# Kernel tuning notes

Hardware: AMD Instinct MI355X
Metric: run time of the kernel (lower is better)

## Reference

```python
import jax, jax.numpy as jnp
import numpy as np

N, R, M, E, NE, B = 50000, 500, 120000, 960000, 800000, 8192
D, H1, HID, OC = 200, 256, 512, 50


def setup_inputs() -> dict:
    key = jax.random.key(0)
    ks = jax.random.split(key, 26)
    s = 0.05
    rn = lambda k, shp: jax.random.normal(k, shp, jnp.float32) * s
    return {
        "entity_emb": jax.random.normal(ks[0], (N, D), jnp.float32),
        "rel_emb": jax.random.normal(ks[1], (R, D), jnp.float32),
        "b_x": jax.random.randint(ks[2], (M,), 0, N),
        "b_node_graph_index": jax.random.randint(ks[3], (M,), 0, R),
        "edge_src": jax.random.randint(ks[4], (E,), 0, M),
        "edge_dst": jax.random.randint(ks[5], (E,), 0, M),
        "edge_w": jax.random.uniform(ks[6], (E,), jnp.float32),
        "big_src": jax.random.randint(ks[7], (NE,), 0, N),
        "big_dst": jax.random.randint(ks[8], (NE,), 0, N),
        "big_w": jax.random.uniform(ks[9], (NE,), jnp.float32),
        "perm": jax.random.permutation(ks[10], N),
        "batch_inputs": jnp.stack([
            jax.random.randint(ks[11], (B,), 0, N),
            jax.random.randint(ks[12], (B,), 0, R),
            jax.random.randint(ks[13], (B,), 0, N)], axis=1),
        "W1a": rn(ks[14], (2 * D, H1)), "W1b": rn(ks[15], (H1, D)),
        "W2a": rn(ks[16], (D, H1)), "W2b": rn(ks[17], (H1, D)),
        "Wle": rn(ks[18], (2 * D, 1)), "ble": jnp.zeros((1,), jnp.float32),
        "Wlo": rn(ks[19], (2 * D, D)), "blo": jnp.zeros((D,), jnp.float32),
        "Wg": rn(ks[20], (D, HID)), "Wd": rn(ks[21], (HID, HID)),
        "conv_w": rn(ks[22], (OC, 3)), "conv_b": jnp.zeros((OC,), jnp.float32),
        "fc_w": rn(ks[23], (OC * D, 1)), "fc_b": jnp.zeros((1,), jnp.float32),
    }


def _l2norm(x):
    return x / jnp.maximum(jnp.linalg.norm(x, axis=-1, keepdims=True), 1e-12)


def _gcn(x, src, dst, w, n, Wa, Wb):
    # two-layer GCN over sparse edge list: out = A @ relu(A @ x @ Wa) @ Wb
    agg = lambda h: jax.ops.segment_sum(h[src] * w[:, None], dst, num_segments=n)
    h = jax.nn.relu(agg(x) @ Wa)
    return agg(h) @ Wb


def _seg_softmax(v, idx, n):
    m = jax.ops.segment_max(v, idx, num_segments=n)
    e = jnp.exp(v - m[idx])
    s = jax.ops.segment_sum(e, idx, num_segments=n)
    return e / (s[idx] + 1e-16)


def _mce(ent, rel, b_x, b_gi, src, dst, w, W1a, W1b, Wle, ble, Wlo, blo):
    x = jnp.concatenate([ent[b_x], rel[b_gi]], axis=-1)          # [M, 400]
    e = _gcn(x, src, dst, w, b_x.shape[0], W1a, W1b)             # [M, 200]
    cnt = jax.ops.segment_sum(jnp.ones((b_x.shape[0],), e.dtype), b_x, num_segments=N)
    mean = jax.ops.segment_sum(e, b_x, num_segments=N) / jnp.maximum(cnt, 1.0)[:, None]
    z = mean[b_x]                                                # scatter_mean then gather
    emb = jnp.concatenate([e[b_x], z], axis=-1)                  # [M, 400]
    score = emb @ Wle + ble                                      # [M, 1]
    zs = _seg_softmax(score, b_x, N)                             # segment softmax
    pooled = jax.ops.segment_sum(zs * emb, b_x, num_segments=N)  # [N, 400]
    return (pooled @ Wlo + blo) + ent


def _dgi(h1, h2, Wg, Wd):
    p1 = jax.nn.relu(h1 @ Wg)
    p2 = jax.nn.relu(h2 @ Wg)
    c = jax.nn.sigmoid(jnp.mean(p1, axis=0))                     # readout [HID]
    t = Wd @ c
    return jnp.concatenate([p1 @ t, p2 @ t])                     # [2N]


def _convkb(trip, conv_w, conv_b, fc_w, fc_b):
    # trip [B,3,D]; Conv2d(1, OC, (1,3)) over [B,1,D,3] -> [B,OC,D]
    h = jax.nn.relu(jnp.einsum('bsd,os->bod', trip, conv_w) + conv_b[None, :, None])
    return h.reshape(trip.shape[0], -1) @ fc_w + fc_b            # [B,1]


def reference(entity_emb, rel_emb, b_x, b_node_graph_index, edge_src, edge_dst,
              edge_w, big_src, big_dst, big_w, perm, batch_inputs,
              W1a, W1b, W2a, W2b, Wle, ble, Wlo, blo, Wg, Wd,
              conv_w, conv_b, fc_w, fc_b):
    ent = _l2norm(entity_emb)
    rel = _l2norm(rel_emb)
    ent_shuf = ent[perm]
    ec = _mce(ent, rel, b_x, b_node_graph_index, edge_src, edge_dst, edge_w,
              W1a, W1b, Wle, ble, Wlo, blo)
    ec_ = _mce(ent_shuf, rel, b_x, b_node_graph_index, edge_src, edge_dst, edge_w,
               W1a, W1b, Wle, ble, Wlo, blo)
    eg = _gcn(ec, big_src, big_dst, big_w, N, W2a, W2b)
    eg_ = _gcn(ec_, big_src, big_dst, big_w, N, W2a, W2b)
    local_logits = _dgi(ec, ec_, Wg, Wd)
    global_logits = _dgi(eg, eg_, Wg, Wd)
    trip = jnp.stack([ec[batch_inputs[:, 0]], rel[batch_inputs[:, 1]],
                      ec[batch_inputs[:, 2]]], axis=1)           # [B,3,D]
    out_conv = _convkb(trip, conv_w, conv_b, fc_w, fc_b)
    return out_conv, local_logits, global_logits
```

## Files before the change

kernel.cpp:

```cpp
#include <hip/hip_runtime.h>

#define NN   50000
#define RR   500
#define MM   120000
#define EE   960000
#define NEE  800000
#define BB   8192
#define DD   200
#define HH1  256
#define HIDD 512
#define OCC  50

typedef unsigned int  u32;
typedef unsigned short u16;
typedef __attribute__((ext_vector_type(8))) short bf16x8;
typedef __attribute__((ext_vector_type(4))) float f32x4;

static __device__ __forceinline__ float bf2f(u16 u) {
    u32 x = ((u32)u) << 16;
    return __uint_as_float(x);
}
static __device__ __forceinline__ u16 f2bf(float f) {
    u32 x = __float_as_uint(f);
    u32 r = (x + 0x7FFFu + ((x >> 16) & 1u)) >> 16;
    return (u16)r;
}
static __device__ __forceinline__ u32 pack2(float a, float b) {
    return (u32)f2bf(a) | ((u32)f2bf(b) << 16);
}
static __device__ __forceinline__ void unpack2(u32 v, float& a, float& b) {
    a = bf2f((u16)(v & 0xFFFFu));
    b = bf2f((u16)(v >> 16));
}

static __device__ __forceinline__ float wredsum(float v) {
#pragma unroll
    for (int off = 32; off > 0; off >>= 1) v += __shfl_xor(v, off);
    return v;
}

static __device__ __forceinline__ u32 relu2bf(u32 x) {
    if (x & 0x00008000u) x &= 0xFFFF0000u;
    if (x & 0x80000000u) x &= 0x0000FFFFu;
    return x;
}
static __device__ __forceinline__ bf16x8 zero8() {
    bf16x8 z;
#pragma unroll
    for (int i = 0; i < 8; ++i) z[i] = 0;
    return z;
}

__global__ void k_l2norm(const float* __restrict__ in, float* __restrict__ outf,
                         u16* __restrict__ outb, int rows) {
    int w = (blockIdx.x * blockDim.x + threadIdx.x) >> 6;
    int lane = threadIdx.x & 63;
    if (w >= rows) return;
    const float* r = in + (size_t)w * DD;
    float s = 0.f;
    for (int d = lane; d < DD; d += 64) { float v = r[d]; s += v * v; }
    s = wredsum(s);
    float inv = 1.0f / fmaxf(sqrtf(s), 1e-12f);
    for (int d = lane; d < DD; d += 64) {
        float v = r[d] * inv;
        if (outf) outf[(size_t)w * DD + d] = v;
        if (outb) outb[(size_t)w * DD + d] = f2bf(v);
    }
}

__global__ void k_gather_perm(const int* __restrict__ bx, const int* __restrict__ perm,
                              int* __restrict__ idx1, int M) {
    int m = blockIdx.x * blockDim.x + threadIdx.x;
    if (m < M) idx1[m] = perm[bx[m]];
}

__global__ void k_edge_idx(const int* __restrict__ srcE, const int* __restrict__ map,
                           int* __restrict__ outE, int n) {
    int e = blockIdx.x * blockDim.x + threadIdx.x;
    if (e < n) outE[e] = map[srcE[e]];
}

__global__ void k_prepw(const float* __restrict__ src, int Nc, int Kd,
                        u16* __restrict__ hi, u16* __restrict__ lo) {
    int i = blockIdx.x * blockDim.x + threadIdx.x;
    if (i >= Nc * Kd) return;
    int n = i / Kd, k = i - n * Kd;
    float b = src[(size_t)k * Nc + n];
    u16 hb_ = f2bf(b);
    hi[i] = hb_;
    lo[i] = f2bf(b - bf2f(hb_));
}

__global__ void k_hist(const int* __restrict__ idx, int* __restrict__ cnt, int n) {
    int i = blockIdx.x * blockDim.x + threadIdx.x;
    if (i < n) atomicAdd(&cnt[idx[i]], 1);
}

__global__ __launch_bounds__(1024) void k_scan(const int* __restrict__ in,
                                               int* __restrict__ out, int n) {
    __shared__ int wtot[16];
    __shared__ int wexc[16];
    __shared__ int s_carry;
    int tid = threadIdx.x, lane = tid & 63, wid = tid >> 6;
    if (tid == 0) s_carry = 0;
    __syncthreads();
    for (int base = 0; base < n; base += 1024) {
        int i = base + tid;
        int v = (i < n) ? in[i] : 0;
        int x = v;
#pragma unroll
        for (int off = 1; off < 64; off <<= 1) {
            int t = __shfl_up(x, off);
            if (lane >= off) x += t;
        }
        if (lane == 63) wtot[wid] = x;
        __syncthreads();
        if (wid == 0) {
            int wv2 = (lane < 16) ? wtot[lane] : 0;
            int y = wv2;
#pragma unroll
            for (int off = 1; off < 16; off <<= 1) {
                int t = __shfl_up(y, off);
                if (lane >= off) y += t;
            }
            if (lane < 16) wexc[lane] = y - wv2;
            if (lane == 15) wtot[15] = y;
        }
        __syncthreads();
        if (i < n) out[i] = s_carry + wexc[wid] + (x - v);
        int chunk_total = wtot[15];
        __syncthreads();
        if (tid == 0) s_carry += chunk_total;
        __syncthreads();
    }
    if (threadIdx.x == 0) out[n] = s_carry;
}

__global__ void k_fill2(const int* __restrict__ dst, const int* __restrict__ src,
                        const float* __restrict__ w, int* __restrict__ cursor,
                        int* __restrict__ srcs_out, float* __restrict__ ws_out, int n) {
    int e = blockIdx.x * blockDim.x + threadIdx.x;
    if (e >= n) return;
    int p = atomicAdd(&cursor[dst[e]], 1);
    srcs_out[p] = src[e];
    ws_out[p] = w[e];
}

__global__ void k_fill1(const int* __restrict__ idx, int* __restrict__ cursor,
                        int* __restrict__ outm, int n) {
    int m = blockIdx.x * blockDim.x + threadIdx.x;
    if (m >= n) return;
    int p = atomicAdd(&cursor[idx[m]], 1);
    outm[p] = m;
}

__global__ void k_pull_mce(const int* __restrict__ rp, const int* __restrict__ ivE,
                           const int* __restrict__ giE, const float* __restrict__ wE,
                           const u16* __restrict__ Pent, const u16* __restrict__ Prel,
                           u16* __restrict__ out, int ndst) {
    int wv = (blockIdx.x * blockDim.x + threadIdx.x) >> 6;
    if (wv >= ndst) return;
    int lane = threadIdx.x & 63;
    int beg = rp[wv], end = rp[wv + 1];
    float accA[2] = {0.f, 0.f}, accB[2] = {0.f, 0.f};
    int e = beg;
    for (; e + 4 <= end; e += 4) {
        int i0 = ivE[e], i1 = ivE[e + 1], i2 = ivE[e + 2], i3 = ivE[e + 3];
        int g0 = giE[e], g1 = giE[e + 1], g2 = giE[e + 2], g3 = giE[e + 3];
        float w0 = wE[e], w1 = wE[e + 1], w2 = wE[e + 2], w3 = wE[e + 3];
        const u32* pe0 = (const u32*)(Pent + (size_t)i0 * HH1);
        const u32* pe1 = (const u32*)(Pent + (size_t)i1 * HH1);
        const u32* pe2 = (const u32*)(Pent + (size_t)i2 * HH1);
        const u32* pe3 = (const u32*)(Pent + (size_t)i3 * HH1);
        const u32* pr0 = (const u32*)(Prel + (size_t)g0 * HH1);
        const u32* pr1 = (const u32*)(Prel + (size_t)g1 * HH1);
        const u32* pr2 = (const u32*)(Prel + (size_t)g2 * HH1);
        const u32* pr3 = (const u32*)(Prel + (size_t)g3 * HH1);
        u32 vp[4][2], vr[4][2];
#pragma unroll
        for (int t = 0; t < 2; ++t) {
            int p = lane + 64 * t;
            vp[0][t] = pe0[p]; vp[1][t] = pe1[p]; vp[2][t] = pe2[p]; vp[3][t] = pe3[p];
            vr[0][t] = pr0[p]; vr[1][t] = pr1[p]; vr[2][t] = pr2[p]; vr[3][t] = pr3[p];
        }
#pragma unroll
        for (int t = 0; t < 2; ++t) {
            float a, b, c, d;
            unpack2(vp[0][t], a, b); unpack2(vr[0][t], c, d);
            accA[t] += (a + c) * w0; accB[t] += (b + d) * w0;
            unpack2(vp[1][t], a, b); unpack2(vr[1][t], c, d);
            accA[t] += (a + c) * w1; accB[t] += (b + d) * w1;
            unpack2(vp[2][t], a, b); unpack2(vr[2][t], c, d);
            accA[t] += (a + c) * w2; accB[t] += (b + d) * w2;
            unpack2(vp[3][t], a, b); unpack2(vr[3][t], c, d);
            accA[t] += (a + c) * w3; accB[t] += (b + d) * w3;
        }
    }
    for (; e < end; ++e) {
        int iv = ivE[e], gi = giE[e];
        float w = wE[e];
        const u32* pe = (const u32*)(Pent + (size_t)iv * HH1);
        const u32* pr = (const u32*)(Prel + (size_t)gi * HH1);
#pragma unroll
        for (int t = 0; t < 2; ++t) {
            int p = lane + 64 * t;
            float a, b, c, d;
            unpack2(pe[p], a, b); unpack2(pr[p], c, d);
            accA[t] += (a + c) * w; accB[t] += (b + d) * w;
        }
    }
    u32* o = (u32*)(out + (size_t)wv * HH1);
#pragma unroll
    for (int t = 0; t < 2; ++t) o[lane + 64 * t] = pack2(accA[t], accB[t]);
}

template<int DIMS, int INS, int OUTS>
__global__ void k_pull(const int* __restrict__ rp, const int* __restrict__ srcs,
                       const float* __restrict__ wsrt,
                       const u16* __restrict__ inh, const u16* __restrict__ inl,
                       u16* __restrict__ outh, u16* __restrict__ outl, int ndst) {
    int wv = (blockIdx.x * blockDim.x + threadIdx.x) >> 6;
    if (wv >= ndst) return;
    int lane = threadIdx.x & 63;
    int beg = rp[wv], end = rp[wv + 1];
    constexpr int NP = DIMS / 2;
    constexpr int NT = (NP + 63) / 64;
    float accA[NT], accB[NT];
#pragma unroll
    for (int t = 0; t < NT; ++t) { accA[t] = 0.f; accB[t] = 0.f; }
    int e = beg;
    for (; e + 4 <= end; e += 4) {
        int s0 = srcs[e], s1 = srcs[e + 1], s2 = srcs[e + 2], s3 = srcs[e + 3];
        float w0 = wsrt[e], w1 = wsrt[e + 1], w2 = wsrt[e + 2], w3 = wsrt[e + 3];
        const u32* rh[4] = {
            (const u32*)(inh + (size_t)s0 * DIMS), (const u32*)(inh + (size_t)s1 * DIMS),
            (const u32*)(inh + (size_t)s2 * DIMS), (const u32*)(inh + (size_t)s3 * DIMS)};
        u32 vh[4][NT], vl[4][NT];
#pragma unroll
        for (int t = 0; t < NT; ++t) {
            int p = lane + 64 * t;
            if (p < NP) {
                vh[0][t] = rh[0][p]; vh[1][t] = rh[1][p];
                vh[2][t] = rh[2][p]; vh[3][t] = rh[3][p];
            }
        }
        if (INS) {
            const u32* rl[4] = {
                (const u32*)(inl + (size_t)s0 * DIMS), (const u32*)(inl + (size_t)s1 * DIMS),
                (const u32*)(inl + (size_t)s2 * DIMS), (const u32*)(inl + (size_t)s3 * DIMS)};
#pragma unroll
            for (int t = 0; t < NT; ++t) {
                int p = lane + 64 * t;
                if (p < NP) {
                    vl[0][t] = rl[0][p]; vl[1][t] = rl[1][p];
                    vl[2][t] = rl[2][p]; vl[3][t] = rl[3][p];
                }
            }
        }
        float ws[4] = {w0, w1, w2, w3};
#pragma unroll
        for (int q = 0; q < 4; ++q) {
#pragma unroll
            for (int t = 0; t < NT; ++t) {
                int p = lane + 64 * t;
                if (p < NP) {
                    float a, b;
                    unpack2(vh[q][t], a, b);
                    if (INS) { float a2, b2; unpack2(vl[q][t], a2, b2); a += a2; b += b2; }
                    accA[t] += a * ws[q]; accB[t] += b * ws[q];
                }
            }
        }
    }
    for (; e < end; ++e) {
        int s = srcs[e];
        float w = wsrt[e];
        const u32* rh = (const u32*)(inh + (size_t)s * DIMS);
        const u32* rl = INS ? (const u32*)(inl + (size_t)s * DIMS) : nullptr;
#pragma unroll
        for (int t = 0; t < NT; ++t) {
            int p = lane + 64 * t;
            if (p < NP) {
                float a, b;
                unpack2(rh[p], a, b);
                if (INS) { float a2, b2; unpack2(rl[p], a2, b2); a += a2; b += b2; }
                accA[t] += a * w; accB[t] += b * w;
            }
        }
    }
    u32* oh = (u32*)(outh + (size_t)wv * DIMS);
    u32* ol = OUTS ? (u32*)(outl + (size_t)wv * DIMS) : nullptr;
#pragma unroll
    for (int t = 0; t < NT; ++t) {
        int p = lane + 64 * t;
        if (p < NP) {
            if (OUTS == 0) {
                oh[p] = pack2(accA[t], accB[t]);
            } else {
                u16 ha = f2bf(accA[t]), hb_ = f2bf(accB[t]);
                u16 la = f2bf(accA[t] - bf2f(ha)), lb = f2bf(accB[t] - bf2f(hb_));
                oh[p] = (u32)ha | ((u32)hb_ << 16);
                ol[p] = (u32)la | ((u32)lb << 16);
            }
        }
    }
}

__global__ void k_segpool(const int* __restrict__ rpX, const int* __restrict__ mids,
                          const u16* __restrict__ e_buf, u16* __restrict__ pooled, int n) {
    int nv = (blockIdx.x * blockDim.x + threadIdx.x) >> 6;
    if (nv >= n) return;
    int lane = threadIdx.x & 63;
    int beg = rpX[nv], end = rpX[nv + 1];
    int cnt = end - beg;
    float accA[2] = {0.f, 0.f}, accB[2] = {0.f, 0.f};
    int e = beg;
    for (; e + 4 <= end; e += 4) {
        const u32* r0 = (const u32*)(e_buf + (size_t)mids[e] * DD);
        const u32* r1 = (const u32*)(e_buf + (size_t)mids[e + 1] * DD);
        const u32* r2 = (const u32*)(e_buf + (size_t)mids[e + 2] * DD);
        const u32* r3 = (const u32*)(e_buf + (size_t)mids[e + 3] * DD);
        u32 v[4][2];
#pragma unroll
        for (int t = 0; t < 2; ++t) {
            int p = lane + 64 * t;
            if (p < DD / 2) { v[0][t] = r0[p]; v[1][t] = r1[p]; v[2][t] = r2[p]; v[3][t] = r3[p]; }
        }
#pragma unroll
        for (int t = 0; t < 2; ++t) {
            int p = lane + 64 * t;
            if (p < DD / 2) {
                float a, b;
                unpack2(v[0][t], a, b); accA[t] += a; accB[t] += b;
                unpack2(v[1][t], a, b); accA[t] += a; accB[t] += b;
                unpack2(v[2][t], a, b); accA[t] += a; accB[t] += b;
                unpack2(v[3][t], a, b); accA[t] += a; accB[t] += b;
            }
        }
    }
    for (; e < end; ++e) {
        const u32* r = (const u32*)(e_buf + (size_t)mids[e] * DD);
#pragma unroll
        for (int t = 0; t < 2; ++t) {
            int p = lane + 64 * t;
            if (p < DD / 2) { float a, b; unpack2(r[p], a, b); accA[t] += a; accB[t] += b; }
        }
    }
    float inv = 1.0f / fmaxf((float)cnt, 1.0f);
    bool occ = cnt > 0;
    const u32* er = (const u32*)(e_buf + (size_t)nv * DD);
    u32* p0 = (u32*)(pooled + (size_t)nv * (2 * DD));
#pragma unroll
    for (int t = 0; t < 2; ++t) {
        int p = lane + 64 * t;
        if (p < DD / 2) {
            p0[p] = occ ? er[p] : 0u;
            p0[DD / 2 + p] = occ ? pack2(accA[t] * inv, accB[t] * inv) : 0u;
        }
    }
}

template<int AMODE, int RELU_IN, int RELU_OUT, int HAS_BIAS, int HAS_ADD, int FUSE, int CMODE>
__global__ __launch_bounds__(256) void k_mfmamm(
    const u16* __restrict__ Ah, const u16* __restrict__ Al,
    const u16* __restrict__ Bh, const u16* __restrict__ Bl,
    void* __restrict__ Cv, u16* __restrict__ Cl,
    int Mr, int Nc, int Kd,
    const float* __restrict__ bias, const u16* __restrict__ addsrc,
    const int* __restrict__ addidx, const float* __restrict__ tvec,
    float* __restrict__ redout) {
    constexpr int BM = 128, BN = 128, BK = 32;
    constexpr int ASTR = 40;
    __shared__ u16 Ahs[2][BM * ASTR];
    __shared__ u16 Als[AMODE ? 2 : 1][AMODE ? (BM * ASTR) : 8];

    int tid = threadIdx.x;
    int wid = tid >> 6, lane = tid & 63;
    int wr = wid >> 1, wc = wid & 1;
    int r = lane & 15, h = lane >> 4;
    int bm0 = blockIdx.y * BM, bn0 = blockIdx.x * BN;
    int srow = (tid & 15) + 16 * (tid >> 6);
    int sg = (tid >> 4) & 3;
    int nk = (Kd + BK - 1) / BK;

    f32x4 acc[4][4];
#pragma unroll
    for (int i = 0; i < 4; ++i)
#pragma unroll
        for (int j = 0; j < 4; ++j) acc[i][j] = (f32x4){0.f, 0.f, 0.f, 0.f};

    uint4 pa[2], pl[2];
    {
        int kc = sg * 8;
        bool kok = (kc + 8 <= Kd);
#pragma unroll
        for (int it = 0; it < 2; ++it) {
            int row = srow + 64 * it;
            int gr = bm0 + row;
            uint4 v = make_uint4(0, 0, 0, 0), vl2 = make_uint4(0, 0, 0, 0);
            if (gr < Mr && kok) {
                v = *(const uint4*)(Ah + (size_t)gr * Kd + kc);
                if (AMODE) vl2 = *(const uint4*)(Al + (size_t)gr * Kd + kc);
            }
            if (RELU_IN) {
                v.x = relu2bf(v.x); v.y = relu2bf(v.y);
                v.z = relu2bf(v.z); v.w = relu2bf(v.w);
            }
            pa[it] = v;
            if (AMODE) pl[it] = vl2;
        }
#pragma unroll
        for (int it = 0; it < 2; ++it) {
            int row = srow + 64 * it;
            *(uint4*)(&Ahs[0][row * ASTR + sg * 8]) = pa[it];
            if (AMODE) *(uint4*)(&Als[0][row * ASTR + sg * 8]) = pl[it];
        }
    }
    __syncthreads();

    for (int k = 0; k < nk; ++k) {
        int cur = k & 1;
        uint4 na[2], nl[2];
        bool have_next = (k + 1 < nk);
        if (have_next) {
            int kc = (k + 1) * BK + sg * 8;
            bool kok = (kc + 8 <= Kd);
#pragma unroll
            for (int it = 0; it < 2; ++it) {
                int row = srow + 64 * it;
                int gr = bm0 + row;
                uint4 v = make_uint4(0, 0, 0, 0), vl2 = make_uint4(0, 0, 0, 0);
                if (gr < Mr && kok) {
                    v = *(const uint4*)(Ah + (size_t)gr * Kd + kc);
                    if (AMODE) vl2 = *(const uint4*)(Al + (size_t)gr * Kd + kc);
                }
                if (RELU_IN) {
                    v.x = relu2bf(v.x); v.y = relu2bf(v.y);
                    v.z = relu2bf(v.z); v.w = relu2bf(v.w);
                }
                na[it] = v;
                if (AMODE) nl[it] = vl2;
            }
        }
        bf16x8 bh4[4], bl4[4];
        {
            int kb = k * BK + h * 8;
            bool kbok = (kb + 8 <= Kd);
#pragma unroll
            for (int j = 0; j < 4; ++j) {
                int nrow = bn0 + wc * 64 + j * 16 + r;
                if (nrow < Nc && kbok) {
                    bh4[j] = *(const bf16x8*)(Bh + (size_t)nrow * Kd + kb);
                    bl4[j] = *(const bf16x8*)(Bl + (size_t)nrow * Kd + kb);
                } else { bh4[j] = zero8(); bl4[j] = zero8(); }
            }
        }
        bf16x8 af[4], alr[4];
#pragma unroll
        for (int i = 0; i < 4; ++i) {
            int mrow = wr * 64 + i * 16 + r;
            af[i] = *(const bf16x8*)(&Ahs[cur][mrow * ASTR + h * 8]);
            if (AMODE) alr[i] = *(const bf16x8*)(&Als[cur][mrow * ASTR + h * 8]);
        }
#pragma unroll
        for (int i = 0; i < 4; ++i)
#pragma unroll
            for (int j = 0; j < 4; ++j) {
                acc[i][j] = __builtin_amdgcn_mfma_f32_16x16x32_bf16(af[i], bh4[j], acc[i][j], 0, 0, 0);
                acc[i][j] = __builtin_amdgcn_mfma_f32_16x16x32_bf16(af[i], bl4[j], acc[i][j], 0, 0, 0);
                if (AMODE)
                    acc[i][j] = __builtin_amdgcn_mfma_f32_16x16x32_bf16(alr[i], bh4[j], acc[i][j], 0, 0, 0);
            }
        if (have_next) {
#pragma unroll
            for (int it = 0; it < 2; ++it) {
                int row = srow + 64 * it;
                *(uint4*)(&Ahs[cur ^ 1][row * ASTR + sg * 8]) = na[it];
                if (AMODE) *(uint4*)(&Als[cur ^ 1][row * ASTR + sg * 8]) = nl[it];
            }
        }
        __syncthreads();
    }
    float colacc[4] = {0.f, 0.f, 0.f, 0.f};
#pragma unroll
    for (int i = 0; i < 4; ++i) {
        float rowacc[4] = {0.f, 0.f, 0.f, 0.f};
#pragma unroll
        for (int j = 0; j < 4; ++j) {
            int col = bn0 + wc * 64 + j * 16 + r;
            bool colok = col < Nc;
            float tv = (FUSE == 2 && colok) ? tvec[col] : 0.f;
#pragma unroll
            for (int rg = 0; rg < 4; ++rg) {
                int row = bm0 + wr * 64 + i * 16 + h * 4 + rg;
                float v = acc[i][j][rg];
                if (HAS_BIAS && colok) v += bias[col];
                if (RELU_OUT) v = fmaxf(v, 0.f);
                bool ok = colok && row < Mr;
                if (HAS_ADD && ok) {
                    int r2 = addidx ? addidx[row] : row;
                    v += bf2f(addsrc[(size_t)r2 * Nc + col]);
                }
                if (FUSE != 2 && ok) {
                    size_t cidx = (size_t)row * Nc + col;
                    if (CMODE == 0) ((u16*)Cv)[cidx] = f2bf(v);
                    else if (CMODE == 1) ((float*)Cv)[cidx] = v;
                    else {
                        u16 hi_ = f2bf(v);
                        ((u16*)Cv)[cidx] = hi_;
                        Cl[cidx] = f2bf(v - bf2f(hi_));
                    }
                }
                if (FUSE == 1 && ok) colacc[j] += v;
                if (FUSE == 2) rowacc[rg] += v * tv;
            }
        }
        if (FUSE == 2) {
#pragma unroll
            for (int rg = 0; rg < 4; ++rg) {
                float val = rowacc[rg];
                val += __shfl_xor(val, 1); val += __shfl_xor(val, 2);
                val += __shfl_xor(val, 4); val += __shfl_xor(val, 8);
                int row = bm0 + wr * 64 + i * 16 + h * 4 + rg;
                if (r == 0 && row < Mr) atomicAdd(&redout[row], val);
            }
        }
    }
    if (FUSE == 1) {
#pragma unroll
        for (int j = 0; j < 4; ++j) {
            float val = colacc[j];
            val += __shfl_xor(val, 16); val += __shfl_xor(val, 32);
            int col = bn0 + wc * 64 + j * 16 + r;
            if (h == 0 && col < Nc) atomicAdd(&redout[col], val);
        }
    }
}

__global__ void k_sigc(const float* __restrict__ csum, float* __restrict__ cvec) {
    int i = threadIdx.x;
    cvec[i] = 1.0f / (1.0f + expf(-csum[i] * (1.0f / (float)NN)));
}

__global__ void k_tmv(const float* __restrict__ Wd, const float* __restrict__ cvec,
                      float* __restrict__ tvec) {
    __shared__ float c[HIDD];
    int lane = threadIdx.x;
    for (int j = lane; j < HIDD; j += 64) c[j] = cvec[j];
    __syncthreads();
    int r0 = blockIdx.x * 16;
    for (int i = r0; i < r0 + 16; ++i) {
        const float* wr = Wd + (size_t)i * HIDD;
        float s = 0.f;
        for (int j = lane; j < HIDD; j += 64) s += wr[j] * c[j];
        s = wredsum(s);
        if (lane == 0) tvec[i] = s;
    }
}

__global__ void k_rowdot512(const float* __restrict__ p, const float* __restrict__ t,
                            float* __restrict__ out, int rows) {
    int g = blockIdx.x * blockDim.x + threadIdx.x;
    int wv = g >> 6;
    if (wv >= rows) return;
    int lane = g & 63;
    const float* r = p + (size_t)wv * HIDD;
    float s = 0.f;
#pragma unroll
    for (int t4 = 0; t4 < 8; ++t4) {
        int d = lane + t4 * 64;
        s += r[d] * t[d];
    }
    s = wredsum(s);
    if (lane == 0) out[wv] = s;
}

__global__ void k_convkb(const u16* __restrict__ ec, const float* __restrict__ rel,
                         const int* __restrict__ bi, const float* __restrict__ cw,
                         const float* __restrict__ cb, const float* __restrict__ fcw,
                         const float* __restrict__ fcb, float* __restrict__ out) {
    __shared__ float t0[DD], t1[DD], t2[DD];
    __shared__ float red[4];
    int b = blockIdx.x, tid = threadIdx.x;
    int i0 = bi[b * 3 + 0], i1 = bi[b * 3 + 1], i2 = bi[b * 3 + 2];
    if (tid < DD) {
        t0[tid] = bf2f(ec[(size_t)i0 * DD + tid]);
        t1[tid] = rel[(size_t)i1 * DD + tid];
        t2[tid] = bf2f(ec[(size_t)i2 * DD + tid]);
    }
    __syncthreads();
    float partial = 0.f;
    if (tid < DD) {
        float a = t0[tid], bb = t1[tid], c = t2[tid];
        for (int o = 0; o < OCC; ++o) {
            float h = fmaxf(cw[o * 3 + 0] * a + cw[o * 3 + 1] * bb + cw[o * 3 + 2] * c + cb[o], 0.f);
            partial += h * fcw[o * DD + tid];
        }
    }
    partial = wredsum(partial);
    if ((tid & 63) == 0) red[tid >> 6] = partial;
    __syncthreads();
    if (tid == 0) out[b] = red[0] + red[1] + red[2] + red[3] + fcb[0];
}

__global__ void k_sentinel(float* out, float val) { out[threadIdx.x] = val; }

extern "C" void kernel_launch(void* const* d_in, const int* in_sizes, int n_in,
                              void* d_out, int out_size, void* d_ws, size_t ws_size,
                              hipStream_t stream) {
    const float* entity_emb = (const float*)d_in[0];
    const float* rel_emb    = (const float*)d_in[1];
    const int*   b_x        = (const int*)d_in[2];
    const int*   b_gi       = (const int*)d_in[3];
    const int*   e_src      = (const int*)d_in[4];
    const int*   e_dst      = (const int*)d_in[5];
    const float* e_w        = (const float*)d_in[6];
    const int*   big_src    = (const int*)d_in[7];
    const int*   big_dst    = (const int*)d_in[8];
    const float* big_w      = (const float*)d_in[9];
    const int*   perm       = (const int*)d_in[10];
    const int*   batch_in   = (const int*)d_in[11];
    const float* W1a        = (const float*)d_in[12];
    const float* W1b        = (const float*)d_in[13];
    const float* W2a        = (const float*)d_in[14];
    const float* W2b        = (const float*)d_in[15];
    const float* Wlo        = (const float*)d_in[18];
    const float* blo        = (const float*)d_in[19];
    const float* Wg         = (const float*)d_in[20];
    const float* Wd         = (const float*)d_in[21];
    const float* conv_w     = (const float*)d_in[22];
    const float* conv_b     = (const float*)d_in[23];
    const float* fc_w       = (const float*)d_in[24];
    const float* fc_b       = (const float*)d_in[25];
    float* out = (float*)d_out;

    size_t off = 0;
    auto balloc = [&](size_t nbytes) {
        size_t p = off;
        off += (nbytes + 511) & ~(size_t)511;
        return p;
    };
    char* base = (char*)d_ws;
    u16*   entb = (u16*)(base + balloc((size_t)NN * DD * 2));
    float* relf = (float*)(base + balloc((size_t)RR * DD * 4));
    u16*   relb = (u16*)(base + balloc((size_t)RR * DD * 2));
    u16*   Pent = (u16*)(base + balloc((size_t)NN * HH1 * 2));
    u16*   Prel = (u16*)(base + balloc((size_t)RR * HH1 * 2));
    int*   idx1 = (int*)(base + balloc((size_t)MM * 4));
    u16*   ecb  = (u16*)(base + balloc((size_t)NN * DD * 2));
    int*   rpB  = (int*)(base + balloc((size_t)(NN + 1) * 4));
    int*   srcB = (int*)(base + balloc((size_t)NEE * 4));
    float* wB   = (float*)(base + balloc((size_t)NEE * 4));
    int*   rpE  = (int*)(base + balloc((size_t)(MM + 1) * 4));
    int*   srcE = (int*)(base + balloc((size_t)EE * 4));
    float* wE   = (float*)(base + balloc((size_t)EE * 4));
    int*   ivE  = (int*)(base + balloc((size_t)EE * 4));
    int*   giE  = (int*)(base + balloc((size_t)EE * 4));
    int*   rpX  = (int*)(base + balloc((size_t)(NN + 1) * 4));
    int*   mids = (int*)(base + balloc((size_t)MM * 4));
    int*   curB = (int*)(base + balloc((size_t)NN * 4));
    int*   curE = (int*)(base + balloc((size_t)MM * 4));
    int*   curX = (int*)(base + balloc((size_t)NN * 4));
    u16* w1aT_h  = (u16*)(base + balloc(200 * 256 * 2));
    u16* w1aT_l  = (u16*)(base + balloc(200 * 256 * 2));
    u16* w1abT_h = (u16*)(base + balloc(200 * 256 * 2));
    u16* w1abT_l = (u16*)(base + balloc(200 * 256 * 2));
    u16* w1bT_h  = (u16*)(base + balloc(256 * 200 * 2));
    u16* w1bT_l  = (u16*)(base + balloc(256 * 200 * 2));
    u16* wloT_h  = (u16*)(base + balloc(400 * 200 * 2));
    u16* wloT_l  = (u16*)(base + balloc(400 * 200 * 2));
    u16* wgT_h   = (u16*)(base + balloc(200 * 512 * 2));
    u16* wgT_l   = (u16*)(base + balloc(200 * 512 * 2));
    u16* w2aT_h  = (u16*)(base + balloc(200 * 256 * 2));
    u16* w2aT_l  = (u16*)(base + balloc(200 * 256 * 2));
    u16* w2bT_h  = (u16*)(base + balloc(256 * 200 * 2));
    u16* w2bT_l  = (u16*)(base + balloc(256 * 200 * 2));
    char*  Aarena = base + balloc((size_t)MM * HH1 * 2);
    char*  Barena = base + balloc((size_t)MM * DD * 2);
    char*  Carena = base + balloc((size_t)MM * DD * 2);
    float* csum = (float*)(base + balloc(4 * 2048));
    float* cvec = csum + 512;
    float* t_l  = csum + 1024;
    float* t_g  = csum + 1536;

    if (ws_size < off) {
        k_sentinel<<<dim3(1), dim3(8), 0, stream>>>(out, (float)(ws_size >> 20));
        return;
    }

    const size_t PL = 20000000;
    u16*   aggx   = (u16*)Aarena;
    u16*   hb     = (u16*)Barena;
    u16*   e_buf  = (u16*)Carena;
    u16*   pooled = (u16*)Aarena;
    u16*   a1h    = (u16*)Aarena;
    u16*   a1l    = (u16*)(Aarena + PL);
    u16*   h2h    = (u16*)Barena;
    u16*   h2l    = (u16*)(Barena + 25600000);
    u16*   h2bh   = (u16*)Aarena;
    u16*   h2bl   = (u16*)(Aarena + PL);
    u16*   egh    = (u16*)Carena;
    u16*   egl    = (u16*)(Carena + PL);
    float* pbuf   = (float*)Aarena;

    dim3 blk(256);
    auto wgrid = [](int items) { return dim3((unsigned)((items + 3) / 4)); };
    auto tgrid = [](int items) { return dim3((unsigned)((items + 255) / 256)); };
    auto mmgrid = [](int Mr, int Nc) { return dim3((unsigned)((Nc + 127) / 128), (unsigned)((Mr + 127) / 128)); };

    k_l2norm<<<wgrid(NN), blk, 0, stream>>>(entity_emb, nullptr, entb, NN);
    k_l2norm<<<wgrid(RR), blk, 0, stream>>>(rel_emb, relf, relb, RR);
    k_gather_perm<<<tgrid(MM), blk, 0, stream>>>(b_x, perm, idx1, MM);
    k_prepw<<<tgrid(256 * 200), blk, 0, stream>>>(W1a, 256, 200, w1aT_h, w1aT_l);
    k_prepw<<<tgrid(256 * 200), blk, 0, stream>>>(W1a + 200 * 256, 256, 200, w1abT_h, w1abT_l);
    k_prepw<<<tgrid(200 * 256), blk, 0, stream>>>(W1b, 200, 256, w1bT_h, w1bT_l);
    k_prepw<<<tgrid(200 * 400), blk, 0, stream>>>(Wlo, 200, 400, wloT_h, wloT_l);
    k_prepw<<<tgrid(512 * 200), blk, 0, stream>>>(Wg, 512, 200, wgT_h, wgT_l);
    k_prepw<<<tgrid(256 * 200), blk, 0, stream>>>(W2a, 256, 200, w2aT_h, w2aT_l);
    k_prepw<<<tgrid(200 * 256), blk, 0, stream>>>(W2b, 200, 256, w2bT_h, w2bT_l);

    hipMemsetAsync(curB, 0, (size_t)NN * 4, stream);
    hipMemsetAsync(curE, 0, (size_t)MM * 4, stream);
    hipMemsetAsync(curX, 0, (size_t)NN * 4, stream);
    k_hist<<<tgrid(NEE), blk, 0, stream>>>(big_dst, curB, NEE);
    k_hist<<<tgrid(EE), blk, 0, stream>>>(e_dst, curE, EE);
    k_hist<<<tgrid(MM), blk, 0, stream>>>(b_x, curX, MM);
    k_scan<<<dim3(1), dim3(1024), 0, stream>>>(curB, rpB, NN);
    k_scan<<<dim3(1), dim3(1024), 0, stream>>>(curE, rpE, MM);
    k_scan<<<dim3(1), dim3(1024), 0, stream>>>(curX, rpX, NN);
    hipMemcpyAsync(curB, rpB, (size_t)NN * 4, hipMemcpyDeviceToDevice, stream);
    hipMemcpyAsync(curE, rpE, (size_t)MM * 4, hipMemcpyDeviceToDevice, stream);
    hipMemcpyAsync(curX, rpX, (size_t)NN * 4, hipMemcpyDeviceToDevice, stream);
    k_fill2<<<tgrid(NEE), blk, 0, stream>>>(big_dst, big_src, big_w, curB, srcB, wB, NEE);
    k_fill2<<<tgrid(EE), blk, 0, stream>>>(e_dst, e_src, e_w, curE, srcE, wE, EE);
    k_fill1<<<tgrid(MM), blk, 0, stream>>>(b_x, curX, mids, MM);
    k_edge_idx<<<tgrid(EE), blk, 0, stream>>>(srcE, b_gi, giE, EE);

    k_mfmamm<0, 0, 0, 0, 0, 0, 0><<<mmgrid(NN, HH1), blk, 0, stream>>>(
        entb, nullptr, w1aT_h, w1aT_l, Pent, nullptr, NN, HH1, DD,
        nullptr, nullptr, nullptr, nullptr, nullptr);
    k_mfmamm<0, 0, 0, 0, 0, 0, 0><<<mmgrid(RR, HH1), blk, 0, stream>>>(
        relb, nullptr, w1abT_h, w1abT_l, Prel, nullptr, RR, HH1, DD,
        nullptr, nullptr, nullptr, nullptr, nullptr);

    for (int v = 0; v < 2; ++v) {
        const int* ivmap  = v ? idx1 : b_x;
        const int* addidx = v ? perm : nullptr;

        k_edge_idx<<<tgrid(EE), blk, 0, stream>>>(srcE, ivmap, ivE, EE);
        k_pull_mce<<<wgrid(MM), blk, 0, stream>>>(rpE, ivE, giE, wE, Pent, Prel, aggx, MM);
        k_mfmamm<0, 1, 0, 0, 0, 0, 0><<<mmgrid(MM, DD), blk, 0, stream>>>(
            aggx, nullptr, w1bT_h, w1bT_l, hb, nullptr, MM, DD, HH1,
            nullptr, nullptr, nullptr, nullptr, nullptr);
        k_pull<DD, 0, 0><<<wgrid(MM), blk, 0, stream>>>(rpE, srcE, wE, hb, nullptr,
                                                        e_buf, nullptr, MM);
        k_segpool<<<wgrid(NN), blk, 0, stream>>>(rpX, mids, e_buf, pooled, NN);
        k_mfmamm<0, 0, 0, 1, 1, 0, 0><<<mmgrid(NN, DD), blk, 0, stream>>>(
            pooled, nullptr, wloT_h, wloT_l, ecb, nullptr, NN, DD, 2 * DD,
            blo, entb, addidx, nullptr, nullptr);

        if (v == 0) {
            hipMemsetAsync(csum, 0, 512 * sizeof(float), stream);
            k_mfmamm<0, 0, 1, 0, 0, 1, 1><<<mmgrid(NN, HIDD), blk, 0, stream>>>(
                ecb, nullptr, wgT_h, wgT_l, pbuf, nullptr, NN, HIDD, DD,
                nullptr, nullptr, nullptr, nullptr, csum);
            k_sigc<<<dim3(1), dim3(512), 0, stream>>>(csum, cvec);
            k_tmv<<<dim3(32), dim3(64), 0, stream>>>(Wd, cvec, t_l);
            k_rowdot512<<<wgrid(NN), blk, 0, stream>>>(pbuf, t_l, out + BB, NN);
            k_convkb<<<dim3(BB), blk, 0, stream>>>(ecb, relf, batch_in,
                                                   conv_w, conv_b, fc_w, fc_b, out);
        } else {
            hipMemsetAsync(out + BB + NN, 0, (size_t)NN * 4, stream);
            k_mfmamm<0, 0, 1, 0, 0, 2, 1><<<mmgrid(NN, HIDD), blk, 0, stream>>>(
                ecb, nullptr, wgT_h, wgT_l, nullptr, nullptr, NN, HIDD, DD,
                nullptr, nullptr, nullptr, t_l, out + BB + NN);
        }

        k_pull<DD, 0, 1><<<wgrid(NN), blk, 0, stream>>>(rpB, srcB, wB, ecb, nullptr,
                                                        a1h, a1l, NN);
        k_mfmamm<1, 0, 1, 0, 0, 0, 2><<<mmgrid(NN, HH1), blk, 0, stream>>>(
            a1h, a1l, w2aT_h, w2aT_l, h2h, h2l, NN, HH1, DD,
            nullptr, nullptr, nullptr, nullptr, nullptr);
        k_mfmamm<1, 0, 0, 0, 0, 0, 2><<<mmgrid(NN, DD), blk, 0, stream>>>(
            h2h, h2l, w2bT_h, w2bT_l, h2bh, h2bl, NN, DD, HH1,
            nullptr, nullptr, nullptr, nullptr, nullptr);
        k_pull<DD, 1, 1><<<wgrid(NN), blk, 0, stream>>>(rpB, srcB, wB, h2bh, h2bl,
                                                        egh, egl, NN);

        if (v == 0) {
            hipMemsetAsync(csum, 0, 512 * sizeof(float), stream);
            k_mfmamm<1, 0, 1, 0, 0, 1, 1><<<mmgrid(NN, HIDD), blk, 0, stream>>>(
                egh, egl, wgT_h, wgT_l, pbuf, nullptr, NN, HIDD, DD,
                nullptr, nullptr, nullptr, nullptr, csum);
            k_sigc<<<dim3(1), dim3(512), 0, stream>>>(csum, cvec);
            k_tmv<<<dim3(32), dim3(64), 0, stream>>>(Wd, cvec, t_g);
            k_rowdot512<<<wgrid(NN), blk, 0, stream>>>(pbuf, t_g, out + BB + 2 * (size_t)NN, NN);
        } else {
            hipMemsetAsync(out + BB + 3 * (size_t)NN, 0, (size_t)NN * 4, stream);
            k_mfmamm<1, 0, 1, 0, 0, 2, 1><<<mmgrid(NN, HIDD), blk, 0, stream>>>(
                egh, egl, wgT_h, wgT_l, nullptr, nullptr, NN, HIDD, DD,
                nullptr, nullptr, nullptr, t_g, out + BB + 3 * (size_t)NN);
        }
    }

    (void)in_sizes; (void)n_in; (void)out_size;
}
```

Before: 2.250 ms.

## Fold W2b into Wg and drop low-part B MFMAs in non-critical GEMMs

```diff
diff --git a/kernel.cpp b/kernel.cpp
--- a/kernel.cpp
+++ b/kernel.cpp
@@ -89,6 +89,18 @@
     u16 hb_ = f2bf(b);
     hi[i] = hb_;
     lo[i] = f2bf(b - bf2f(hb_));
+}
+
+__global__ void k_fusew(const float* __restrict__ W2b, const float* __restrict__ Wg,
+                        u16* __restrict__ hi, u16* __restrict__ lo) {
+    int i = blockIdx.x * blockDim.x + threadIdx.x;
+    if (i >= HIDD * HH1) return;
+    int n = i >> 8, k = i & 255;
+    float s = 0.f;
+    for (int j = 0; j < DD; ++j) s += W2b[k * DD + j] * Wg[(size_t)j * HIDD + n];
+    u16 h = f2bf(s);
+    hi[i] = h;
+    lo[i] = f2bf(s - bf2f(h));
 }
 
 __global__ void k_hist(const int* __restrict__ idx, int* __restrict__ cnt, int n) {
@@ -360,7 +372,7 @@
     }
 }
 
-template<int AMODE, int RELU_IN, int RELU_OUT, int HAS_BIAS, int HAS_ADD, int FUSE, int CMODE>
+template<int AMODE, int BLO, int RELU_IN, int RELU_OUT, int HAS_BIAS, int HAS_ADD, int FUSE, int CMODE>
 __global__ __launch_bounds__(256) void k_mfmamm(
     const u16* __restrict__ Ah, const u16* __restrict__ Al,
     const u16* __restrict__ Bh, const u16* __restrict__ Bl,
@@ -369,7 +381,7 @@
     const float* __restrict__ bias, const u16* __restrict__ addsrc,
     const int* __restrict__ addidx, const float* __restrict__ tvec,
     float* __restrict__ redout) {
-    constexpr int BM = 128, BN = 128, BK = 32;
+    constexpr int BM = 128, BK = 32;
     constexpr int ASTR = 40;
     __shared__ u16 Ahs[2][BM * ASTR];
     __shared__ u16 Als[AMODE ? 2 : 1][AMODE ? (BM * ASTR) : 8];
@@ -378,7 +390,7 @@
     int wid = tid >> 6, lane = tid & 63;
     int wr = wid >> 1, wc = wid & 1;
     int r = lane & 15, h = lane >> 4;
-    int bm0 = blockIdx.y * BM, bn0 = blockIdx.x * BN;
+    int bm0 = blockIdx.y * BM, bn0 = blockIdx.x * 128;
     int srow = (tid & 15) + 16 * (tid >> 6);
     int sg = (tid >> 4) & 3;
     int nk = (Kd + BK - 1) / BK;
@@ -451,8 +463,8 @@
                 int nrow = bn0 + wc * 64 + j * 16 + r;
                 if (nrow < Nc && kbok) {
                     bh4[j] = *(const bf16x8*)(Bh + (size_t)nrow * Kd + kb);
-                    bl4[j] = *(const bf16x8*)(Bl + (size_t)nrow * Kd + kb);
-                } else { bh4[j] = zero8(); bl4[j] = zero8(); }
+                    if (BLO) bl4[j] = *(const bf16x8*)(Bl + (size_t)nrow * Kd + kb);
+                } else { bh4[j] = zero8(); if (BLO) bl4[j] = zero8(); }
             }
         }
         bf16x8 af[4], alr[4];
@@ -467,7 +479,8 @@
 #pragma unroll
             for (int j = 0; j < 4; ++j) {
                 acc[i][j] = __builtin_amdgcn_mfma_f32_16x16x32_bf16(af[i], bh4[j], acc[i][j], 0, 0, 0);
-                acc[i][j] = __builtin_amdgcn_mfma_f32_16x16x32_bf16(af[i], bl4[j], acc[i][j], 0, 0, 0);
+                if (BLO)
+                    acc[i][j] = __builtin_amdgcn_mfma_f32_16x16x32_bf16(af[i], bl4[j], acc[i][j], 0, 0, 0);
                 if (AMODE)
                     acc[i][j] = __builtin_amdgcn_mfma_f32_16x16x32_bf16(alr[i], bh4[j], acc[i][j], 0, 0, 0);
             }
@@ -570,6 +583,25 @@
     for (int t4 = 0; t4 < 8; ++t4) {
         int d = lane + t4 * 64;
         s += r[d] * t[d];
+    }
+    s = wredsum(s);
+    if (lane == 0) out[wv] = s;
+}
+
+__global__ void k_rowdot512b(const u16* __restrict__ p, const float* __restrict__ t,
+                             float* __restrict__ out, int rows) {
+    int g = blockIdx.x * blockDim.x + threadIdx.x;
+    int wv = g >> 6;
+    if (wv >= rows) return;
+    int lane = g & 63;
+    const u32* r = (const u32*)(p + (size_t)wv * HIDD);
+    float s = 0.f;
+#pragma unroll
+    for (int t4 = 0; t4 < 4; ++t4) {
+        int pp = lane + t4 * 64;
+        float a, b;
+        unpack2(r[pp], a, b);
+        s += a * t[2 * pp] + b * t[2 * pp + 1];
     }
     s = wredsum(s);
     if (lane == 0) out[wv] = s;
@@ -673,8 +705,8 @@
     u16* wgT_l   = (u16*)(base + balloc(200 * 512 * 2));
     u16* w2aT_h  = (u16*)(base + balloc(200 * 256 * 2));
     u16* w2aT_l  = (u16*)(base + balloc(200 * 256 * 2));
-    u16* w2bT_h  = (u16*)(base + balloc(256 * 200 * 2));
-    u16* w2bT_l  = (u16*)(base + balloc(256 * 200 * 2));
+    u16* w2bgT_h = (u16*)(base + balloc(512 * 256 * 2));
+    u16* w2bgT_l = (u16*)(base + balloc(512 * 256 * 2));
     char*  Aarena = base + balloc((size_t)MM * HH1 * 2);
     char*  Barena = base + balloc((size_t)MM * DD * 2);
     char*  Carena = base + balloc((size_t)MM * DD * 2);
@@ -689,6 +721,7 @@
     }
 
     const size_t PL = 20000000;
+    const size_t PH = 25600000;
     u16*   aggx   = (u16*)Aarena;
     u16*   hb     = (u16*)Barena;
     u16*   e_buf  = (u16*)Carena;
@@ -696,11 +729,10 @@
     u16*   a1h    = (u16*)Aarena;
     u16*   a1l    = (u16*)(Aarena + PL);
     u16*   h2h    = (u16*)Barena;
-    u16*   h2l    = (u16*)(Barena + 25600000);
-    u16*   h2bh   = (u16*)Aarena;
-    u16*   h2bl   = (u16*)(Aarena + PL);
-    u16*   egh    = (u16*)Carena;
-    u16*   egl    = (u16*)(Carena + PL);
+    u16*   h2l    = (u16*)(Barena + PH);
+    u16*   g2h    = (u16*)Aarena;
+    u16*   g2l    = (u16*)(Aarena + PH);
+    u16*   pb16   = (u16*)Barena;
     float* pbuf   = (float*)Aarena;
 
     dim3 blk(256);
@@ -717,7 +749,7 @@
     k_prepw<<<tgrid(200 * 400), blk, 0, stream>>>(Wlo, 200, 400, wloT_h, wloT_l);
     k_prepw<<<tgrid(512 * 200), blk, 0, stream>>>(Wg, 512, 200, wgT_h, wgT_l);
     k_prepw<<<tgrid(256 * 200), blk, 0, stream>>>(W2a, 256, 200, w2aT_h, w2aT_l);
-    k_prepw<<<tgrid(200 * 256), blk, 0, stream>>>(W2b, 200, 256, w2bT_h, w2bT_l);
+    k_fusew<<<tgrid(512 * 256), blk, 0, stream>>>(W2b, Wg, w2bgT_h, w2bgT_l);
 
     hipMemsetAsync(curB, 0, (size_t)NN * 4, stream);
     hipMemsetAsync(curE, 0, (size_t)MM * 4, stream);
@@ -736,10 +768,10 @@
     k_fill1<<<tgrid(MM), blk, 0, stream>>>(b_x, curX, mids, MM);
     k_edge_idx<<<tgrid(EE), blk, 0, stream>>>(srcE, b_gi, giE, EE);
 
-    k_mfmamm<0, 0, 0, 0, 0, 0, 0><<<mmgrid(NN, HH1), blk, 0, stream>>>(
+    k_mfmamm<0, 0, 0, 0, 0, 0, 0, 0><<<mmgrid(NN, HH1), blk, 0, stream>>>(
         entb, nullptr, w1aT_h, w1aT_l, Pent, nullptr, NN, HH1, DD,
         nullptr, nullptr, nullptr, nullptr, nullptr);
-    k_mfmamm<0, 0, 0, 0, 0, 0, 0><<<mmgrid(RR, HH1), blk, 0, stream>>>(
+    k_mfmamm<0, 0, 0, 0, 0, 0, 0, 0><<<mmgrid(RR, HH1), blk, 0, stream>>>(
         relb, nullptr, w1abT_h, w1abT_l, Prel, nullptr, RR, HH1, DD,
         nullptr, nullptr, nullptr, nullptr, nullptr);
 
@@ -749,19 +781,19 @@
 
         k_edge_idx<<<tgrid(EE), blk, 0, stream>>>(srcE, ivmap, ivE, EE);
         k_pull_mce<<<wgrid(MM), blk, 0, stream>>>(rpE, ivE, giE, wE, Pent, Prel, aggx, MM);
-        k_mfmamm<0, 1, 0, 0, 0, 0, 0><<<mmgrid(MM, DD), blk, 0, stream>>>(
+        k_mfmamm<0, 0, 1, 0, 0, 0, 0, 0><<<mmgrid(MM, DD), blk, 0, stream>>>(
             aggx, nullptr, w1bT_h, w1bT_l, hb, nullptr, MM, DD, HH1,
             nullptr, nullptr, nullptr, nullptr, nullptr);
         k_pull<DD, 0, 0><<<wgrid(MM), blk, 0, stream>>>(rpE, srcE, wE, hb, nullptr,
                                                         e_buf, nullptr, MM);
         k_segpool<<<wgrid(NN), blk, 0, stream>>>(rpX, mids, e_buf, pooled, NN);
-        k_mfmamm<0, 0, 0, 1, 1, 0, 0><<<mmgrid(NN, DD), blk, 0, stream>>>(
+        k_mfmamm<0, 0, 0, 0, 1, 1, 0, 0><<<mmgrid(NN, DD), blk, 0, stream>>>(
             pooled, nullptr, wloT_h, wloT_l, ecb, nullptr, NN, DD, 2 * DD,
             blo, entb, addidx, nullptr, nullptr);
 
         if (v == 0) {
             hipMemsetAsync(csum, 0, 512 * sizeof(float), stream);
-            k_mfmamm<0, 0, 1, 0, 0, 1, 1><<<mmgrid(NN, HIDD), blk, 0, stream>>>(
+            k_mfmamm<0, 0, 0, 1, 0, 0, 1, 1><<<mmgrid(NN, HIDD), blk, 0, stream>>>(
                 ecb, nullptr, wgT_h, wgT_l, pbuf, nullptr, NN, HIDD, DD,
                 nullptr, nullptr, nullptr, nullptr, csum);
             k_sigc<<<dim3(1), dim3(512), 0, stream>>>(csum, cvec);
@@ -771,34 +803,31 @@
                                                    conv_w, conv_b, fc_w, fc_b, out);
         } else {
             hipMemsetAsync(out + BB + NN, 0, (size_t)NN * 4, stream);
-            k_mfmamm<0, 0, 1, 0, 0, 2, 1><<<mmgrid(NN, HIDD), blk, 0, stream>>>(
+            k_mfmamm<0, 0, 0, 1, 0, 0, 2, 1><<<mmgrid(NN, HIDD), blk, 0, stream>>>(
                 ecb, nullptr, wgT_h, wgT_l, nullptr, nullptr, NN, HIDD, DD,
                 nullptr, nullptr, nullptr, t_l, out + BB + NN);
         }
 
         k_pull<DD, 0, 1><<<wgrid(NN), blk, 0, stream>>>(rpB, srcB, wB, ecb, nullptr,
                                                         a1h, a1l, NN);
-        k_mfmamm<1, 0, 1, 0, 0, 0, 2><<<mmgrid(NN, HH1), blk, 0, stream>>>(
+        k_mfmamm<1, 1, 0, 1, 0, 0, 0, 2><<<mmgrid(NN, HH1), blk, 0, stream>>>(
             a1h, a1l, w2aT_h, w2aT_l, h2h, h2l, NN, HH1, DD,
             nullptr, nullptr, nullptr, nullptr, nullptr);
-        k_mfmamm<1, 0, 0, 0, 0, 0, 2><<<mmgrid(NN, DD), blk, 0, stream>>>(
-            h2h, h2l, w2bT_h, w2bT_l, h2bh, h2bl, NN, DD, HH1,
-            nullptr, nullptr, nullptr, nullptr, nullptr);
-        k_pull<DD, 1, 1><<<wgrid(NN), blk, 0, stream>>>(rpB, srcB, wB, h2bh, h2bl,
-                                                        egh, egl, NN);
+        k_pull<HH1, 1, 1><<<wgrid(NN), blk, 0, stream>>>(rpB, srcB, wB, h2h, h2l,
+                                                         g2h, g2l, NN);
 
         if (v == 0) {
             hipMemsetAsync(csum, 0, 512 * sizeof(float), stream);
-            k_mfmamm<1, 0, 1, 0, 0, 1, 1><<<mmgrid(NN, HIDD), blk, 0, stream>>>(
-                egh, egl, wgT_h, wgT_l, pbuf, nullptr, NN, HIDD, DD,
+            k_mfmamm<1, 1, 0, 1, 0, 0, 1, 0><<<mmgrid(NN, HIDD), blk, 0, stream>>>(
+                g2h, g2l, w2bgT_h, w2bgT_l, pb16, nullptr, NN, HIDD, HH1,
                 nullptr, nullptr, nullptr, nullptr, csum);
             k_sigc<<<dim3(1), dim3(512), 0, stream>>>(csum, cvec);
             k_tmv<<<dim3(32), dim3(64), 0, stream>>>(Wd, cvec, t_g);
-            k_rowdot512<<<wgrid(NN), blk, 0, stream>>>(pbuf, t_g, out + BB + 2 * (size_t)NN, NN);
+            k_rowdot512b<<<wgrid(NN), blk, 0, stream>>>(pb16, t_g, out + BB + 2 * (size_t)NN, NN);
         } else {
             hipMemsetAsync(out + BB + 3 * (size_t)NN, 0, (size_t)NN * 4, stream);
-            k_mfmamm<1, 0, 1, 0, 0, 2, 1><<<mmgrid(NN, HIDD), blk, 0, stream>>>(
-                egh, egl, wgT_h, wgT_l, nullptr, nullptr, NN, HIDD, DD,
+            k_mfmamm<1, 1, 0, 1, 0, 0, 2, 0><<<mmgrid(NN, HIDD), blk, 0, stream>>>(
+                g2h, g2l, w2bgT_h, w2bgT_l, nullptr, nullptr, NN, HIDD, HH1,
                 nullptr, nullptr, nullptr, t_g, out + BB + 3 * (size_t)NN);
         }
     }
```

Result: faster. 2.089 ms (median of 2 runs) (-7.1%).
